# Optimization experiments

Measured on AMD Instinct MI355X. Metric: run time of the kernel, lower is better.

## Reference

```python
import jax, jax.numpy as jnp
import numpy as np
from jax import lax

H = 64          # GRU hidden size
OUT_STEPS = 20  # output_seq_size


def _maxpool2(x):
    # x: [N, C, H, W] -> 2x2 max pool, stride 2, VALID
    return lax.reduce_window(x, -jnp.inf, lax.max, (1, 1, 2, 2), (1, 1, 2, 2), 'VALID')


def _conv(x, w, b):
    # NCHW / OIHW, VALID, stride 1
    y = lax.conv_general_dilated(x, w, (1, 1), 'VALID',
                                 dimension_numbers=('NCHW', 'OIHW', 'NCHW'))
    return y + b[None, :, None, None]


def _gru_step(h, x, wih, whh, bih, bhh):
    # PyTorch GRU gate order: r, z, n
    gi = x @ wih.T + bih            # [B, 3H]
    gh = h @ whh.T + bhh            # [B, 3H]
    i_r, i_z, i_n = jnp.split(gi, 3, axis=-1)
    h_r, h_z, h_n = jnp.split(gh, 3, axis=-1)
    r = jax.nn.sigmoid(i_r + h_r)
    z = jax.nn.sigmoid(i_z + h_z)
    n = jnp.tanh(i_n + r * h_n)
    return (1.0 - z) * n + z * h


def setup_inputs() -> dict:
    key = jax.random.key(0)
    ks = jax.random.split(key, 20)
    B, T = 1024, 31
    s = 0.1
    return {
        'bbox_seq': jax.random.normal(ks[0], (B, T, 4), jnp.float32),
        'head_seq': jax.random.uniform(ks[1], (B, T, 32, 32), jnp.float32),
        'conv1_w': jax.random.normal(ks[2], (4, 1, 3, 3), jnp.float32) * s,
        'conv1_b': jax.random.normal(ks[3], (4,), jnp.float32) * s,
        'conv2_w': jax.random.normal(ks[4], (10, 4, 3, 3), jnp.float32) * s,
        'conv2_b': jax.random.normal(ks[5], (10,), jnp.float32) * s,
        'fc_w': jax.random.normal(ks[6], (5, 360), jnp.float32) * s,
        'fc_b': jax.random.normal(ks[7], (5,), jnp.float32) * s,
        'enc_wih': jax.random.normal(ks[8], (3 * H, 9), jnp.float32) * s,
        'enc_whh': jax.random.normal(ks[9], (3 * H, H), jnp.float32) * s,
        'enc_bih': jax.random.normal(ks[10], (3 * H,), jnp.float32) * s,
        'enc_bhh': jax.random.normal(ks[11], (3 * H,), jnp.float32) * s,
        'dec_wih': jax.random.normal(ks[12], (3 * H, 4), jnp.float32) * s,
        'dec_whh': jax.random.normal(ks[13], (3 * H, H), jnp.float32) * s,
        'dec_bih': jax.random.normal(ks[14], (3 * H,), jnp.float32) * s,
        'dec_bhh': jax.random.normal(ks[15], (3 * H,), jnp.float32) * s,
        'lin_w': jax.random.normal(ks[16], (4, H), jnp.float32) * s,
        'lin_b': jax.random.normal(ks[17], (4,), jnp.float32) * s,
    }


def reference(bbox_seq, head_seq, conv1_w, conv1_b, conv2_w, conv2_b, fc_w, fc_b,
              enc_wih, enc_whh, enc_bih, enc_bhh,
              dec_wih, dec_whh, dec_bih, dec_bhh, lin_w, lin_b):
    B, T = bbox_seq.shape[0], bbox_seq.shape[1]
    L = T - 1  # encoder sequence length

    # offset: last bbox, broadcast over OUT_STEPS -> [B, OUT_STEPS, 4]
    offset = jnp.broadcast_to(bbox_seq[:, -1][:, None, :], (B, OUT_STEPS, 4))

    diffs = bbox_seq[:, 1:] - bbox_seq[:, :-1]  # [B, L, 4] (dropout p=0 -> identity)

    # --- ConvEncoder on all head crops at once ---
    imgs = head_seq[:, :-1].reshape(B * L, 1, 32, 32)
    x = jax.nn.relu(_conv(imgs, conv1_w, conv1_b))   # [BL, 4, 30, 30]
    x = _maxpool2(x)                                  # [BL, 4, 15, 15]
    x = jax.nn.relu(_conv(x, conv2_w, conv2_b))       # [BL, 10, 13, 13]
    x = _maxpool2(x)                                  # [BL, 10, 6, 6]
    emb = x.reshape(B * L, -1) @ fc_w.T + fc_b        # [BL, 5]
    emb = emb.reshape(B, L, -1)

    enc_in = jnp.concatenate([diffs, emb], axis=2)    # [B, L, 9]

    # --- GRU encoder (scan over time) ---
    def enc_step(h, x_t):
        h = _gru_step(h, x_t, enc_wih, enc_whh, enc_bih, enc_bhh)
        return h, None
    h0 = jnp.zeros((B, H), enc_in.dtype)
    hn, _ = lax.scan(enc_step, h0, jnp.swapaxes(enc_in, 0, 1))

    def dec_step(carry, _):
        h, prev_x = carry
        h = _gru_step(h, prev_x, dec_wih, dec_whh, dec_bih, dec_bhh)
        x_new = h @ lin_w.T + lin_b + prev_x
        return (h, x_new), x_new
    (_, _), outs = lax.scan(dec_step, (hn, diffs[:, -1]), None, length=OUT_STEPS)
    out = jnp.swapaxes(outs, 0, 1)                    # [B, OUT_STEPS, 4]

    return jnp.cumsum(out, axis=1) + offset
```

## Files before the change

kernel.cpp:

```cpp
#include <hip/hip_runtime.h>
#include <hip/hip_bf16.h>


#define B_    1024
#define L_    30
#define H_    64

typedef _Float16 half_t;
typedef __attribute__((ext_vector_type(8))) _Float16 half8;
typedef __attribute__((ext_vector_type(4))) float f32x4;

#define MFMA16(A, B, C) __builtin_amdgcn_mfma_f32_16x16x32_f16(A, B, C, 0, 0, 0)

__device__ __forceinline__ float sigmoid_f(float v) {
    return __builtin_amdgcn_rcpf(1.f + __expf(-v));
}
__device__ __forceinline__ float tanh_f(float v) {
    v = fminf(fmaxf(v, -15.f), 15.f);
    const float e = __expf(2.f * v);
    return (e - 1.f) * __builtin_amdgcn_rcpf(e + 1.f);
}
__device__ __forceinline__ void load4_lds(float* r, const float* p) {
    float2 a = *(const float2*)p;
    float2 b = *(const float2*)(p + 2);
    r[0] = a.x; r[1] = a.y; r[2] = b.x; r[3] = b.y;
}

__global__ __launch_bounds__(64) void conv_embed_kernel(
    const float* __restrict__ bbox,
    const float* __restrict__ head,
    const float* __restrict__ c1w, const float* __restrict__ c1b,
    const float* __restrict__ c2w, const float* __restrict__ c2b,
    const float* __restrict__ fcw, const float* __restrict__ fcb,
    float* __restrict__ enc_in)
{
    const int img = blockIdx.x;
    const int b = img / L_;
    const int l = img % L_;
    const int tid = threadIdx.x;

    __shared__ float s_img[32 * 32];
    __shared__ float s_p1[4 * 15 * 16];
    __shared__ float s_p2[360];
    __shared__ float s_red[60];

    {
        const float4* src = (const float4*)(head + ((size_t)b * 31 + (size_t)l) * 1024);
        float4* dst = (float4*)s_img;
        #pragma unroll
        for (int i = 0; i < 4; ++i) dst[tid + 64 * i] = src[tid + 64 * i];
    }
    __syncthreads();

    if (tid < 60) {
        const int c = tid / 15, px = tid % 15;
        const int x0 = 2 * px;
        float wg[9];
        #pragma unroll
        for (int k = 0; k < 9; ++k) wg[k] = c1w[c * 9 + k];
        const float bias = c1b[c];

        auto c1out = [&](const float* ra, const float* rb, const float* rc, const float* rd) -> float {
            float a00 = bias, a01 = bias, a10 = bias, a11 = bias;
            #pragma unroll
            for (int kx = 0; kx < 3; ++kx) {
                const float w0 = wg[kx], w1 = wg[3 + kx], w2 = wg[6 + kx];
                a00 = fmaf(w0, ra[kx],     fmaf(w1, rb[kx],     fmaf(w2, rc[kx],     a00)));
                a01 = fmaf(w0, ra[kx + 1], fmaf(w1, rb[kx + 1], fmaf(w2, rc[kx + 1], a01)));
                a10 = fmaf(w0, rb[kx],     fmaf(w1, rc[kx],     fmaf(w2, rd[kx],     a10)));
                a11 = fmaf(w0, rb[kx + 1], fmaf(w1, rc[kx + 1], fmaf(w2, rd[kx + 1], a11)));
            }
            a00 = fmaxf(a00, 0.f); a01 = fmaxf(a01, 0.f);
            a10 = fmaxf(a10, 0.f); a11 = fmaxf(a11, 0.f);
            return fmaxf(fmaxf(a00, a01), fmaxf(a10, a11));
        };

        float r[6][4];
        load4_lds(r[0], s_img + 0 * 32 + x0);
        load4_lds(r[1], s_img + 1 * 32 + x0);
        #pragma unroll
        for (int i = 0; i < 7; ++i) {
            const int s0 = (4 * i) % 6, s1 = (4 * i + 1) % 6, s2 = (4 * i + 2) % 6;
            const int s3 = (4 * i + 3) % 6, s4 = (4 * i + 4) % 6, s5 = (4 * i + 5) % 6;
            load4_lds(r[s2], s_img + (4 * i + 2) * 32 + x0);
            load4_lds(r[s3], s_img + (4 * i + 3) * 32 + x0);
            s_p1[c * 240 + (2 * i) * 16 + px] = c1out(r[s0], r[s1], r[s2], r[s3]);
            load4_lds(r[s4], s_img + (4 * i + 4) * 32 + x0);
            load4_lds(r[s5], s_img + (4 * i + 5) * 32 + x0);
            s_p1[c * 240 + (2 * i + 1) * 16 + px] = c1out(r[s2], r[s3], r[s4], r[s5]);
        }
        load4_lds(r[0], s_img + 30 * 32 + x0);
        load4_lds(r[1], s_img + 31 * 32 + x0);
        s_p1[c * 240 + 14 * 16 + px] = c1out(r[4], r[5], r[0], r[1]);
    }
    __syncthreads();

    if (tid < 60) {
        const int c = tid / 6, px = tid % 6;
        const int x0 = 2 * px;
        float wg2[4][9];
        #pragma unroll
        for (int ic = 0; ic < 4; ++ic)
            #pragma unroll
            for (int k = 0; k < 9; ++k) wg2[ic][k] = c2w[(c * 4 + ic) * 9 + k];
        const float bias2 = c2b[c];

        float P[6][4][4];
        auto c2out = [&](float (*pa)[4], float (*pb)[4], float (*pc)[4], float (*pd)[4]) -> float {
            float a00 = bias2, a01 = bias2, a10 = bias2, a11 = bias2;
            #pragma unroll
            for (int ic = 0; ic < 4; ++ic) {
                #pragma unroll
                for (int kx = 0; kx < 3; ++kx) {
                    const float w0 = wg2[ic][kx], w1 = wg2[ic][3 + kx], w2 = wg2[ic][6 + kx];
                    a00 = fmaf(w0, pa[ic][kx],     fmaf(w1, pb[ic][kx],     fmaf(w2, pc[ic][kx],     a00)));
                    a01 = fmaf(w0, pa[ic][kx + 1], fmaf(w1, pb[ic][kx + 1], fmaf(w2, pc[ic][kx + 1], a01)));
                    a10 = fmaf(w0, pb[ic][kx],     fmaf(w1, pc[ic][kx],     fmaf(w2, pd[ic][kx],     a10)));
                    a11 = fmaf(w0, pb[ic][kx + 1], fmaf(w1, pc[ic][kx + 1], fmaf(w2, pd[ic][kx + 1], a11)));
                }
            }
            a00 = fmaxf(a00, 0.f); a01 = fmaxf(a01, 0.f);
            a10 = fmaxf(a10, 0.f); a11 = fmaxf(a11, 0.f);
            return fmaxf(fmaxf(a00, a01), fmaxf(a10, a11));
        };

        #pragma unroll
        for (int ic = 0; ic < 4; ++ic) {
            load4_lds(P[0][ic], s_p1 + ic * 240 + 0 * 16 + x0);
            load4_lds(P[1][ic], s_p1 + ic * 240 + 1 * 16 + x0);
        }
        #pragma unroll
        for (int i = 0; i < 3; ++i) {
            const int s0 = (4 * i) % 6, s1 = (4 * i + 1) % 6, s2 = (4 * i + 2) % 6;
            const int s3 = (4 * i + 3) % 6, s4 = (4 * i + 4) % 6, s5 = (4 * i + 5) % 6;
            #pragma unroll
            for (int ic = 0; ic < 4; ++ic) {
                load4_lds(P[s2][ic], s_p1 + ic * 240 + (4 * i + 2) * 16 + x0);
                load4_lds(P[s3][ic], s_p1 + ic * 240 + (4 * i + 3) * 16 + x0);
            }
            s_p2[c * 36 + (2 * i) * 6 + px] = c2out(P[s0], P[s1], P[s2], P[s3]);
            #pragma unroll
            for (int ic = 0; ic < 4; ++ic) {
                load4_lds(P[s4][ic], s_p1 + ic * 240 + (4 * i + 4) * 16 + x0);
                load4_lds(P[s5][ic], s_p1 + ic * 240 + (4 * i + 5) * 16 + x0);
            }
            s_p2[c * 36 + (2 * i + 1) * 6 + px] = c2out(P[s2], P[s3], P[s4], P[s5]);
        }
    }
    __syncthreads();

    if (tid < 60) {
        const int o = tid / 12, i0 = tid % 12;
        const float* wrow = fcw + o * 360;
        float acc = 0.f;
        #pragma unroll
        for (int k = 0; k < 30; ++k) {
            const int i = i0 + 12 * k;
            acc = fmaf(wrow[i], s_p2[i], acc);
        }
        s_red[tid] = acc;
    }
    __syncthreads();

    float* dst = enc_in + ((size_t)b * L_ + l) * 9;
    if (tid < 5) {
        float acc = fcb[tid];
        #pragma unroll
        for (int k = 0; k < 12; ++k) acc += s_red[tid * 12 + k];
        dst[4 + tid] = acc;
    } else if (tid >= 8 && tid < 12) {
        const int d = tid - 8;
        const float* bb = bbox + (size_t)b * 124 + (size_t)l * 4;
        dst[d] = bb[4 + d] - bb[d];
    }
}

__global__ __launch_bounds__(256, 1) void gru_mfma_kernel(
    const float* __restrict__ bbox,
    const float* __restrict__ enc_in,
    const float* __restrict__ ewih, const float* __restrict__ ewhh,
    const float* __restrict__ ebih, const float* __restrict__ ebhh,
    const float* __restrict__ dwih, const float* __restrict__ dwhh,
    const float* __restrict__ dbih, const float* __restrict__ dbhh,
    const float* __restrict__ linw, const float* __restrict__ linb,
    float* __restrict__ out)
{
    const int bb  = blockIdx.x * 16;
    const int tid = threadIdx.x;
    const int w   = tid >> 6;
    const int l   = tid & 63;
    const int q   = l >> 4;
    const int col = l & 15;

    alignas(16) __shared__ half_t hbuf[2][16][72];
    alignas(16) __shared__ half_t xenc[30][16][40];
    alignas(16) __shared__ half_t xdec[16][40];

    {
        int4* p = (int4*)hbuf;
        for (int i = tid; i < (int)(sizeof(hbuf) / 16); i += 256) p[i] = int4{0, 0, 0, 0};
        p = (int4*)xenc;
        for (int i = tid; i < (int)(sizeof(xenc) / 16); i += 256) p[i] = int4{0, 0, 0, 0};
        p = (int4*)xdec;
        for (int i = tid; i < (int)(sizeof(xdec) / 16); i += 256) p[i] = int4{0, 0, 0, 0};
    }
    __syncthreads();

    for (int pr = tid; pr < 480; pr += 256) {
        const int t = pr / 16, b = pr % 16;
        const float* src = enc_in + ((size_t)(bb + b) * L_ + t) * 9;
        #pragma unroll
        for (int d = 0; d < 9; ++d) xenc[t][b][d] = (half_t)src[d];
    }

    float xold[4], ofs[4], cs[4];
    if (w == 0 && col < 4) {
        #pragma unroll
        for (int r = 0; r < 4; ++r) {
            const float* bbp = bbox + (size_t)(bb + q * 4 + r) * 124;
            xold[r] = bbp[120 + col] - bbp[116 + col];
            ofs[r]  = bbp[120 + col];
            cs[r]   = 0.f;
            xdec[q * 4 + r][col] = (half_t)xold[r];
        }
    }

    const int urow = 16 * w + col;
    auto whh_frag = [&](const float* W, int gate, int kap) -> half8 {
        const float* rp = W + (size_t)(gate * 64 + urow) * 64 + kap * 32 + q * 8;
        half8 f;
        #pragma unroll
        for (int j = 0; j < 8; ++j) f[j] = (half_t)rp[j];
        return f;
    };
    auto wih_frag = [&](const float* W, int gate, int indim) -> half8 {
        half8 f;
        #pragma unroll
        for (int j = 0; j < 8; ++j) {
            const int d = q * 8 + j;
            f[j] = (d < indim) ? (half_t)W[(size_t)(gate * 64 + urow) * indim + d]
                               : (half_t)0.f;
        }
        return f;
    };

    const half8 eBr0 = whh_frag(ewhh, 0, 0), eBr1 = whh_frag(ewhh, 0, 1);
    const half8 eBz0 = whh_frag(ewhh, 1, 0), eBz1 = whh_frag(ewhh, 1, 1);
    const half8 eBn0 = whh_frag(ewhh, 2, 0), eBn1 = whh_frag(ewhh, 2, 1);
    const half8 eBrx = wih_frag(ewih, 0, 9);
    const half8 eBzx = wih_frag(ewih, 1, 9);
    const half8 eBnx = wih_frag(ewih, 2, 9);

    const half8 dBr0 = whh_frag(dwhh, 0, 0), dBr1 = whh_frag(dwhh, 0, 1);
    const half8 dBz0 = whh_frag(dwhh, 1, 0), dBz1 = whh_frag(dwhh, 1, 1);
    const half8 dBn0 = whh_frag(dwhh, 2, 0), dBn1 = whh_frag(dwhh, 2, 1);
    const half8 dBrx = wih_frag(dwih, 0, 4);
    const half8 dBzx = wih_frag(dwih, 1, 4);
    const half8 dBnx = wih_frag(dwih, 2, 4);

    half8 Bl0, Bl1;
    #pragma unroll
    for (int j = 0; j < 8; ++j) {
        Bl0[j] = (col < 4) ? (half_t)linw[col * 64 +      q * 8 + j] : (half_t)0.f;
        Bl1[j] = (col < 4) ? (half_t)linw[col * 64 + 32 + q * 8 + j] : (half_t)0.f;
    }

    const float ebr  = ebih[urow]       + ebhh[urow];
    const float ebz  = ebih[64 + urow]  + ebhh[64 + urow];
    const float ebnh = ebhh[128 + urow];
    const float ebni = ebih[128 + urow];
    const float dbr  = dbih[urow]       + dbhh[urow];
    const float dbz  = dbih[64 + urow]  + dbhh[64 + urow];
    const float dbnh = dbhh[128 + urow];
    const float dbni = dbih[128 + urow];
    const float lb   = (col < 4) ? linb[col] : 0.f;

    float hold[4] = {0.f, 0.f, 0.f, 0.f};
    __syncthreads();

    for (int t = 0; t < L_; ++t) {
        const int p = t & 1;
        const half8 a0 = *(const half8*)&hbuf[p][col][q * 8];
        const half8 a1 = *(const half8*)&hbuf[p][col][32 + q * 8];
        const half8 a2 = *(const half8*)&xenc[t][col][q * 8];

        f32x4 Cr  = {ebr, ebr, ebr, ebr};
        f32x4 Cz  = {ebz, ebz, ebz, ebz};
        f32x4 Cnh = {ebnh, ebnh, ebnh, ebnh};
        f32x4 Cnx = {ebni, ebni, ebni, ebni};
        Cr  = MFMA16(a0, eBr0, Cr);  Cr  = MFMA16(a1, eBr1, Cr);  Cr = MFMA16(a2, eBrx, Cr);
        Cz  = MFMA16(a0, eBz0, Cz);  Cz  = MFMA16(a1, eBz1, Cz);  Cz = MFMA16(a2, eBzx, Cz);
        Cnh = MFMA16(a0, eBn0, Cnh); Cnh = MFMA16(a1, eBn1, Cnh);
        Cnx = MFMA16(a2, eBnx, Cnx);

        #pragma unroll
        for (int r = 0; r < 4; ++r) {
            const float rr = sigmoid_f(Cr[r]);
            const float zz = sigmoid_f(Cz[r]);
            const float nn = tanh_f(Cnx[r] + rr * Cnh[r]);
            hold[r] = fmaf(zz, hold[r] - nn, nn);
            hbuf[p ^ 1][q * 4 + r][urow] = (half_t)hold[r];
        }
        __syncthreads();
    }

    for (int tt = 0; tt < 20; ++tt) {
        const int p = tt & 1;
        const half8 a0 = *(const half8*)&hbuf[p][col][q * 8];
        const half8 a1 = *(const half8*)&hbuf[p][col][32 + q * 8];
        const half8 a2 = *(const half8*)&xdec[col][q * 8];

        f32x4 Cr  = {dbr, dbr, dbr, dbr};
        f32x4 Cz  = {dbz, dbz, dbz, dbz};
        f32x4 Cnh = {dbnh, dbnh, dbnh, dbnh};
        f32x4 Cnx = {dbni, dbni, dbni, dbni};
        Cr  = MFMA16(a0, dBr0, Cr);  Cr  = MFMA16(a1, dBr1, Cr);  Cr = MFMA16(a2, dBrx, Cr);
        Cz  = MFMA16(a0, dBz0, Cz);  Cz  = MFMA16(a1, dBz1, Cz);  Cz = MFMA16(a2, dBzx, Cz);
        Cnh = MFMA16(a0, dBn0, Cnh); Cnh = MFMA16(a1, dBn1, Cnh);
        Cnx = MFMA16(a2, dBnx, Cnx);

        #pragma unroll
        for (int r = 0; r < 4; ++r) {
            const float rr = sigmoid_f(Cr[r]);
            const float zz = sigmoid_f(Cz[r]);
            const float nn = tanh_f(Cnx[r] + rr * Cnh[r]);
            hold[r] = fmaf(zz, hold[r] - nn, nn);
            hbuf[p ^ 1][q * 4 + r][urow] = (half_t)hold[r];
        }
        __syncthreads();

        const half8 al0 = *(const half8*)&hbuf[p ^ 1][col][q * 8];
        const half8 al1 = *(const half8*)&hbuf[p ^ 1][col][32 + q * 8];
        f32x4 X = {0.f, 0.f, 0.f, 0.f};
        X = MFMA16(al0, Bl0, X);
        X = MFMA16(al1, Bl1, X);

        if (w == 0 && col < 4) {
            #pragma unroll
            for (int r = 0; r < 4; ++r) {
                const float xv = X[r] + lb + xold[r];
                xold[r] = xv;
                cs[r] += xv;
                xdec[q * 4 + r][col] = (half_t)xv;
                out[(size_t)(bb + q * 4 + r) * 80 + tt * 4 + col] = cs[r] + ofs[r];
            }
        }
        __syncthreads();
    }
}

extern "C" void kernel_launch(void* const* d_in, const int* in_sizes, int n_in,
                              void* d_out, int out_size, void* d_ws, size_t ws_size,
                              hipStream_t stream) {
    (void)in_sizes; (void)n_in; (void)out_size; (void)ws_size;
    const float* bbox = (const float*)d_in[0];
    const float* head = (const float*)d_in[1];
    const float* c1w  = (const float*)d_in[2];
    const float* c1b  = (const float*)d_in[3];
    const float* c2w  = (const float*)d_in[4];
    const float* c2b  = (const float*)d_in[5];
    const float* fcw  = (const float*)d_in[6];
    const float* fcb  = (const float*)d_in[7];
    const float* ewih = (const float*)d_in[8];
    const float* ewhh = (const float*)d_in[9];
    const float* ebih = (const float*)d_in[10];
    const float* ebhh = (const float*)d_in[11];
    const float* dwih = (const float*)d_in[12];
    const float* dwhh = (const float*)d_in[13];
    const float* dbih = (const float*)d_in[14];
    const float* dbhh = (const float*)d_in[15];
    const float* linw = (const float*)d_in[16];
    const float* linb = (const float*)d_in[17];
    float* out = (float*)d_out;

    float* enc_in = (float*)d_ws;

    conv_embed_kernel<<<B_ * L_, 64, 0, stream>>>(bbox, head, c1w, c1b, c2w, c2b,
                                                  fcw, fcb, enc_in);
    gru_mfma_kernel<<<B_ / 16, 256, 0, stream>>>(bbox, enc_in,
                                                 ewih, ewhh, ebih, ebhh,
                                                 dwih, dwhh, dbih, dbhh,
                                                 linw, linb, out);
}
```

Baseline: 284.5 us.

## Run GRU recurrence in a single wavefront per batch tile with wave barriers

```diff
diff --git a/kernel.cpp b/kernel.cpp
--- a/kernel.cpp
+++ b/kernel.cpp
@@ -175,7 +175,7 @@
     }
 }
 
-__global__ __launch_bounds__(256, 1) void gru_mfma_kernel(
+__global__ __launch_bounds__(64, 1) void gru_mfma_kernel(
     const float* __restrict__ bbox,
     const float* __restrict__ enc_in,
     const float* __restrict__ ewih, const float* __restrict__ ewhh,
@@ -185,28 +185,25 @@
     const float* __restrict__ linw, const float* __restrict__ linb,
     float* __restrict__ out)
 {
-    const int bb  = blockIdx.x * 16;
-    const int tid = threadIdx.x;
-    const int w   = tid >> 6;
-    const int l   = tid & 63;
-    const int q   = l >> 4;
-    const int col = l & 15;
-
-    alignas(16) __shared__ half_t hbuf[2][16][72];
+    const int bb   = blockIdx.x * 16;
+    const int lane = threadIdx.x;
+    const int q    = lane >> 4;
+    const int col  = lane & 15;
+
+    alignas(16) __shared__ half_t hA[16][72];
     alignas(16) __shared__ half_t xenc[30][16][40];
     alignas(16) __shared__ half_t xdec[16][40];
 
     {
-        int4* p = (int4*)hbuf;
-        for (int i = tid; i < (int)(sizeof(hbuf) / 16); i += 256) p[i] = int4{0, 0, 0, 0};
+        int4* p = (int4*)hA;
+        for (int i = lane; i < (int)(sizeof(hA) / 16); i += 64) p[i] = int4{0, 0, 0, 0};
         p = (int4*)xenc;
-        for (int i = tid; i < (int)(sizeof(xenc) / 16); i += 256) p[i] = int4{0, 0, 0, 0};
+        for (int i = lane; i < (int)(sizeof(xenc) / 16); i += 64) p[i] = int4{0, 0, 0, 0};
         p = (int4*)xdec;
-        for (int i = tid; i < (int)(sizeof(xdec) / 16); i += 256) p[i] = int4{0, 0, 0, 0};
-    }
-    __syncthreads();
-
-    for (int pr = tid; pr < 480; pr += 256) {
+        for (int i = lane; i < (int)(sizeof(xdec) / 16); i += 64) p[i] = int4{0, 0, 0, 0};
+    }
+
+    for (int pr = lane; pr < 480; pr += 64) {
         const int t = pr / 16, b = pr % 16;
         const float* src = enc_in + ((size_t)(bb + b) * L_ + t) * 9;
         #pragma unroll
@@ -214,7 +211,7 @@
     }
 
     float xold[4], ofs[4], cs[4];
-    if (w == 0 && col < 4) {
+    if (col < 4) {
         #pragma unroll
         for (int r = 0; r < 4; ++r) {
             const float* bbp = bbox + (size_t)(bb + q * 4 + r) * 124;
@@ -224,128 +221,165 @@
             xdec[q * 4 + r][col] = (half_t)xold[r];
         }
     }
-
-    const int urow = 16 * w + col;
-    auto whh_frag = [&](const float* W, int gate, int kap) -> half8 {
-        const float* rp = W + (size_t)(gate * 64 + urow) * 64 + kap * 32 + q * 8;
+    __builtin_amdgcn_wave_barrier();
+
+    auto h_frag = [&](const float* W, int g, int nt, int kap) -> half8 {
+        const float* rp = W + (size_t)(g * 64 + nt * 16 + col) * 64 + kap * 32 + q * 8;
         half8 f;
         #pragma unroll
         for (int j = 0; j < 8; ++j) f[j] = (half_t)rp[j];
         return f;
     };
-    auto wih_frag = [&](const float* W, int gate, int indim) -> half8 {
+    auto x_frag = [&](const float* W, int g, int nt, int indim) -> half8 {
         half8 f;
         #pragma unroll
         for (int j = 0; j < 8; ++j) {
             const int d = q * 8 + j;
-            f[j] = (d < indim) ? (half_t)W[(size_t)(gate * 64 + urow) * indim + d]
+            f[j] = (d < indim) ? (half_t)W[(size_t)(g * 64 + nt * 16 + col) * indim + d]
                                : (half_t)0.f;
         }
         return f;
     };
 
-    const half8 eBr0 = whh_frag(ewhh, 0, 0), eBr1 = whh_frag(ewhh, 0, 1);
-    const half8 eBz0 = whh_frag(ewhh, 1, 0), eBz1 = whh_frag(ewhh, 1, 1);
-    const half8 eBn0 = whh_frag(ewhh, 2, 0), eBn1 = whh_frag(ewhh, 2, 1);
-    const half8 eBrx = wih_frag(ewih, 0, 9);
-    const half8 eBzx = wih_frag(ewih, 1, 9);
-    const half8 eBnx = wih_frag(ewih, 2, 9);
-
-    const half8 dBr0 = whh_frag(dwhh, 0, 0), dBr1 = whh_frag(dwhh, 0, 1);
-    const half8 dBz0 = whh_frag(dwhh, 1, 0), dBz1 = whh_frag(dwhh, 1, 1);
-    const half8 dBn0 = whh_frag(dwhh, 2, 0), dBn1 = whh_frag(dwhh, 2, 1);
-    const half8 dBrx = wih_frag(dwih, 0, 4);
-    const half8 dBzx = wih_frag(dwih, 1, 4);
-    const half8 dBnx = wih_frag(dwih, 2, 4);
-
-    half8 Bl0, Bl1;
+    float hold[4][4];
     #pragma unroll
-    for (int j = 0; j < 8; ++j) {
-        Bl0[j] = (col < 4) ? (half_t)linw[col * 64 +      q * 8 + j] : (half_t)0.f;
-        Bl1[j] = (col < 4) ? (half_t)linw[col * 64 + 32 + q * 8 + j] : (half_t)0.f;
-    }
-
-    const float ebr  = ebih[urow]       + ebhh[urow];
-    const float ebz  = ebih[64 + urow]  + ebhh[64 + urow];
-    const float ebnh = ebhh[128 + urow];
-    const float ebni = ebih[128 + urow];
-    const float dbr  = dbih[urow]       + dbhh[urow];
-    const float dbz  = dbih[64 + urow]  + dbhh[64 + urow];
-    const float dbnh = dbhh[128 + urow];
-    const float dbni = dbih[128 + urow];
-    const float lb   = (col < 4) ? linb[col] : 0.f;
-
-    float hold[4] = {0.f, 0.f, 0.f, 0.f};
-    __syncthreads();
-
-    for (int t = 0; t < L_; ++t) {
-        const int p = t & 1;
-        const half8 a0 = *(const half8*)&hbuf[p][col][q * 8];
-        const half8 a1 = *(const half8*)&hbuf[p][col][32 + q * 8];
-        const half8 a2 = *(const half8*)&xenc[t][col][q * 8];
-
-        f32x4 Cr  = {ebr, ebr, ebr, ebr};
-        f32x4 Cz  = {ebz, ebz, ebz, ebz};
-        f32x4 Cnh = {ebnh, ebnh, ebnh, ebnh};
-        f32x4 Cnx = {ebni, ebni, ebni, ebni};
-        Cr  = MFMA16(a0, eBr0, Cr);  Cr  = MFMA16(a1, eBr1, Cr);  Cr = MFMA16(a2, eBrx, Cr);
-        Cz  = MFMA16(a0, eBz0, Cz);  Cz  = MFMA16(a1, eBz1, Cz);  Cz = MFMA16(a2, eBzx, Cz);
-        Cnh = MFMA16(a0, eBn0, Cnh); Cnh = MFMA16(a1, eBn1, Cnh);
-        Cnx = MFMA16(a2, eBnx, Cnx);
-
-        #pragma unroll
-        for (int r = 0; r < 4; ++r) {
-            const float rr = sigmoid_f(Cr[r]);
-            const float zz = sigmoid_f(Cz[r]);
-            const float nn = tanh_f(Cnx[r] + rr * Cnh[r]);
-            hold[r] = fmaf(zz, hold[r] - nn, nn);
-            hbuf[p ^ 1][q * 4 + r][urow] = (half_t)hold[r];
-        }
-        __syncthreads();
-    }
-
-    for (int tt = 0; tt < 20; ++tt) {
-        const int p = tt & 1;
-        const half8 a0 = *(const half8*)&hbuf[p][col][q * 8];
-        const half8 a1 = *(const half8*)&hbuf[p][col][32 + q * 8];
-        const half8 a2 = *(const half8*)&xdec[col][q * 8];
-
-        f32x4 Cr  = {dbr, dbr, dbr, dbr};
-        f32x4 Cz  = {dbz, dbz, dbz, dbz};
-        f32x4 Cnh = {dbnh, dbnh, dbnh, dbnh};
-        f32x4 Cnx = {dbni, dbni, dbni, dbni};
-        Cr  = MFMA16(a0, dBr0, Cr);  Cr  = MFMA16(a1, dBr1, Cr);  Cr = MFMA16(a2, dBrx, Cr);
-        Cz  = MFMA16(a0, dBz0, Cz);  Cz  = MFMA16(a1, dBz1, Cz);  Cz = MFMA16(a2, dBzx, Cz);
-        Cnh = MFMA16(a0, dBn0, Cnh); Cnh = MFMA16(a1, dBn1, Cnh);
-        Cnx = MFMA16(a2, dBnx, Cnx);
-
-        #pragma unroll
-        for (int r = 0; r < 4; ++r) {
-            const float rr = sigmoid_f(Cr[r]);
-            const float zz = sigmoid_f(Cz[r]);
-            const float nn = tanh_f(Cnx[r] + rr * Cnh[r]);
-            hold[r] = fmaf(zz, hold[r] - nn, nn);
-            hbuf[p ^ 1][q * 4 + r][urow] = (half_t)hold[r];
-        }
-        __syncthreads();
-
-        const half8 al0 = *(const half8*)&hbuf[p ^ 1][col][q * 8];
-        const half8 al1 = *(const half8*)&hbuf[p ^ 1][col][32 + q * 8];
-        f32x4 X = {0.f, 0.f, 0.f, 0.f};
-        X = MFMA16(al0, Bl0, X);
-        X = MFMA16(al1, Bl1, X);
-
-        if (w == 0 && col < 4) {
-            #pragma unroll
-            for (int r = 0; r < 4; ++r) {
-                const float xv = X[r] + lb + xold[r];
-                xold[r] = xv;
-                cs[r] += xv;
-                xdec[q * 4 + r][col] = (half_t)xv;
-                out[(size_t)(bb + q * 4 + r) * 80 + tt * 4 + col] = cs[r] + ofs[r];
-            }
-        }
-        __syncthreads();
+    for (int nt = 0; nt < 4; ++nt)
+        #pragma unroll
+        for (int r = 0; r < 4; ++r) hold[nt][r] = 0.f;
+
+    {
+        half8 eh[3][4][2], ex[3][4];
+        #pragma unroll
+        for (int g = 0; g < 3; ++g)
+            #pragma unroll
+            for (int nt = 0; nt < 4; ++nt) {
+                eh[g][nt][0] = h_frag(ewhh, g, nt, 0);
+                eh[g][nt][1] = h_frag(ewhh, g, nt, 1);
+                ex[g][nt]    = x_frag(ewih, g, nt, 9);
+            }
+        float br[4], bz[4], bnh[4], bni[4];
+        #pragma unroll
+        for (int nt = 0; nt < 4; ++nt) {
+            const int u = nt * 16 + col;
+            br[nt]  = ebih[u]       + ebhh[u];
+            bz[nt]  = ebih[64 + u]  + ebhh[64 + u];
+            bnh[nt] = ebhh[128 + u];
+            bni[nt] = ebih[128 + u];
+        }
+
+        #pragma unroll 1
+        for (int t = 0; t < L_; ++t) {
+            const half8 a0 = *(const half8*)&hA[col][q * 8];
+            const half8 a1 = *(const half8*)&hA[col][32 + q * 8];
+            const half8 a2 = *(const half8*)&xenc[t][col][q * 8];
+
+            #pragma unroll
+            for (int nt = 0; nt < 4; ++nt) {
+                f32x4 Cr  = {br[nt], br[nt], br[nt], br[nt]};
+                f32x4 Cz  = {bz[nt], bz[nt], bz[nt], bz[nt]};
+                f32x4 Cnh = {bnh[nt], bnh[nt], bnh[nt], bnh[nt]};
+                f32x4 Cnx = {bni[nt], bni[nt], bni[nt], bni[nt]};
+                Cr  = MFMA16(a0, eh[0][nt][0], Cr);
+                Cr  = MFMA16(a1, eh[0][nt][1], Cr);
+                Cr  = MFMA16(a2, ex[0][nt],    Cr);
+                Cz  = MFMA16(a0, eh[1][nt][0], Cz);
+                Cz  = MFMA16(a1, eh[1][nt][1], Cz);
+                Cz  = MFMA16(a2, ex[1][nt],    Cz);
+                Cnh = MFMA16(a0, eh[2][nt][0], Cnh);
+                Cnh = MFMA16(a1, eh[2][nt][1], Cnh);
+                Cnx = MFMA16(a2, ex[2][nt],    Cnx);
+
+                #pragma unroll
+                for (int r = 0; r < 4; ++r) {
+                    const float rr = sigmoid_f(Cr[r]);
+                    const float zz = sigmoid_f(Cz[r]);
+                    const float nn = tanh_f(Cnx[r] + rr * Cnh[r]);
+                    hold[nt][r] = fmaf(zz, hold[nt][r] - nn, nn);
+                    hA[q * 4 + r][nt * 16 + col] = (half_t)hold[nt][r];
+                }
+            }
+            __builtin_amdgcn_wave_barrier();
+        }
+    }
+
+    {
+        half8 dh[3][4][2], dx[3][4];
+        #pragma unroll
+        for (int g = 0; g < 3; ++g)
+            #pragma unroll
+            for (int nt = 0; nt < 4; ++nt) {
+                dh[g][nt][0] = h_frag(dwhh, g, nt, 0);
+                dh[g][nt][1] = h_frag(dwhh, g, nt, 1);
+                dx[g][nt]    = x_frag(dwih, g, nt, 4);
+            }
+        float br[4], bz[4], bnh[4], bni[4];
+        #pragma unroll
+        for (int nt = 0; nt < 4; ++nt) {
+            const int u = nt * 16 + col;
+            br[nt]  = dbih[u]       + dbhh[u];
+            bz[nt]  = dbih[64 + u]  + dbhh[64 + u];
+            bnh[nt] = dbhh[128 + u];
+            bni[nt] = dbih[128 + u];
+        }
+        half8 Bl0, Bl1;
+        #pragma unroll
+        for (int j = 0; j < 8; ++j) {
+            Bl0[j] = (col < 4) ? (half_t)linw[col * 64 +      q * 8 + j] : (half_t)0.f;
+            Bl1[j] = (col < 4) ? (half_t)linw[col * 64 + 32 + q * 8 + j] : (half_t)0.f;
+        }
+        const float lb = (col < 4) ? linb[col] : 0.f;
+
+        #pragma unroll 1
+        for (int tt = 0; tt < 20; ++tt) {
+            const half8 a0 = *(const half8*)&hA[col][q * 8];
+            const half8 a1 = *(const half8*)&hA[col][32 + q * 8];
+            const half8 a2 = *(const half8*)&xdec[col][q * 8];
+
+            #pragma unroll
+            for (int nt = 0; nt < 4; ++nt) {
+                f32x4 Cr  = {br[nt], br[nt], br[nt], br[nt]};
+                f32x4 Cz  = {bz[nt], bz[nt], bz[nt], bz[nt]};
+                f32x4 Cnh = {bnh[nt], bnh[nt], bnh[nt], bnh[nt]};
+                f32x4 Cnx = {bni[nt], bni[nt], bni[nt], bni[nt]};
+                Cr  = MFMA16(a0, dh[0][nt][0], Cr);
+                Cr  = MFMA16(a1, dh[0][nt][1], Cr);
+                Cr  = MFMA16(a2, dx[0][nt],    Cr);
+                Cz  = MFMA16(a0, dh[1][nt][0], Cz);
+                Cz  = MFMA16(a1, dh[1][nt][1], Cz);
+                Cz  = MFMA16(a2, dx[1][nt],    Cz);
+                Cnh = MFMA16(a0, dh[2][nt][0], Cnh);
+                Cnh = MFMA16(a1, dh[2][nt][1], Cnh);
+                Cnx = MFMA16(a2, dx[2][nt],    Cnx);
+
+                #pragma unroll
+                for (int r = 0; r < 4; ++r) {
+                    const float rr = sigmoid_f(Cr[r]);
+                    const float zz = sigmoid_f(Cz[r]);
+                    const float nn = tanh_f(Cnx[r] + rr * Cnh[r]);
+                    hold[nt][r] = fmaf(zz, hold[nt][r] - nn, nn);
+                    hA[q * 4 + r][nt * 16 + col] = (half_t)hold[nt][r];
+                }
+            }
+            __builtin_amdgcn_wave_barrier();
+
+            const half8 al0 = *(const half8*)&hA[col][q * 8];
+            const half8 al1 = *(const half8*)&hA[col][32 + q * 8];
+            f32x4 X = {0.f, 0.f, 0.f, 0.f};
+            X = MFMA16(al0, Bl0, X);
+            X = MFMA16(al1, Bl1, X);
+
+            if (col < 4) {
+                #pragma unroll
+                for (int r = 0; r < 4; ++r) {
+                    const float xv = X[r] + lb + xold[r];
+                    xold[r] = xv;
+                    cs[r] += xv;
+                    xdec[q * 4 + r][col] = (half_t)xv;
+                    out[(size_t)(bb + q * 4 + r) * 80 + tt * 4 + col] = cs[r] + ofs[r];
+                }
+            }
+            __builtin_amdgcn_wave_barrier();
+        }
     }
 }
 
@@ -377,8 +411,8 @@
 
     conv_embed_kernel<<<B_ * L_, 64, 0, stream>>>(bbox, head, c1w, c1b, c2w, c2b,
                                                   fcw, fcb, enc_in);
-    gru_mfma_kernel<<<B_ / 16, 256, 0, stream>>>(bbox, enc_in,
-                                                 ewih, ewhh, ebih, ebhh,
-                                                 dwih, dwhh, dbih, dbhh,
-                                                 linw, linb, out);
-}
+    gru_mfma_kernel<<<B_ / 16, 64, 0, stream>>>(bbox, enc_in,
+                                                ewih, ewhh, ebih, ebhh,
+                                                dwih, dwhh, dbih, dbhh,
+                                                linw, linb, out);
+}
```

After: 334.1 us. +17.4%, slower.
